# Optimization experiments

Hardware: AMD Instinct MI355X
Metric: run time of the kernel (lower is better)

The kernel has to match this reference:

```python
import jax, jax.numpy as jnp
import numpy as np

EMBED_DIM = 256
NUM_WEIGHTS = 8
NUM_RELATIONS = 5
BATCH = 131072


def setup_inputs() -> dict:
    key = jax.random.key(0)
    k1, k2, k3, k4 = jax.random.split(key, 4)
    embeds1 = jax.random.normal(k1, (BATCH, EMBED_DIM), dtype=jnp.float32)
    embeds2 = jax.random.normal(k2, (BATCH, EMBED_DIM), dtype=jnp.float32)
    # Embedding(num_weights, D*D): torch default init is N(0,1)
    rel_embeds = jax.random.normal(k3, (NUM_WEIGHTS, EMBED_DIM * EMBED_DIM), dtype=jnp.float32)
    # weight_scalars ~ U(-stdv, stdv), stdv = 1/sqrt(num_relations)
    stdv = 1.0 / np.sqrt(NUM_RELATIONS)
    weight_scalars = jax.random.uniform(
        k4, (NUM_WEIGHTS, NUM_RELATIONS), dtype=jnp.float32, minval=-stdv, maxval=stdv
    )
    return {
        "embeds1": embeds1,
        "embeds2": embeds2,
        "rel_embeds": rel_embeds,
        "weight_scalars": weight_scalars,
    }


def reference(embeds1, embeds2, rel_embeds, weight_scalars):
    D = embeds1.shape[1]
    W = rel_embeds.shape[0]
    rel_mats = rel_embeds.reshape(W, D, D)  # [W, D, D]
    # Fused bilinear form u . R_w . v for every w: [B, W]
    basis_outputs = jnp.einsum("bi,wij,bj->bw", embeds1, rel_mats, embeds2)
    logit = basis_outputs @ weight_scalars  # [B, R]
    return logit
```

## Files before the change

### kernel.cpp

```cpp
#include <hip/hip_runtime.h>
#include <hip/hip_bf16.h>

#define ED   256
#define NW   8
#define NR   5
#define BM   128
#define BCOL 128
#define BK   32
#define NSTEP (NR * 8)

typedef float  f32x4  __attribute__((ext_vector_type(4)));
typedef __bf16 bf16x8 __attribute__((ext_vector_type(8)));
typedef unsigned short u16;

__device__ __forceinline__ u16 f2bf(float f) {
    return __builtin_bit_cast(u16, __float2bfloat16(f));
}

__device__ __forceinline__ bf16x8 pack8(f32x4 a, f32x4 b) {
    union { u16 u[8]; bf16x8 v; } r;
    r.u[0] = f2bf(a[0]); r.u[1] = f2bf(a[1]); r.u[2] = f2bf(a[2]); r.u[3] = f2bf(a[3]);
    r.u[4] = f2bf(b[0]); r.u[5] = f2bf(b[1]); r.u[6] = f2bf(b[2]); r.u[7] = f2bf(b[3]);
    return r.v;
}

__global__ void prep_S(const float* __restrict__ rel,
                       const float* __restrict__ ws,
                       u16* __restrict__ S_T) {
    int idx = blockIdx.x * blockDim.x + threadIdx.x;
    if (idx >= ED * ED) return;
    int i = idx & (ED - 1);
    int j = idx >> 8;
    float acc[NR];
#pragma unroll
    for (int r = 0; r < NR; ++r) acc[r] = 0.f;
#pragma unroll
    for (int w = 0; w < NW; ++w) {
        float rv = rel[(size_t)w * ED * ED + (size_t)i * ED + j];
#pragma unroll
        for (int r = 0; r < NR; ++r) acc[r] += rv * ws[w * NR + r];
    }
#pragma unroll
    for (int r = 0; r < NR; ++r)
        S_T[((size_t)r * ED + j) * ED + i] = f2bf(acc[r]);
}

__global__ __launch_bounds__(256, 2) void bilinear_kernel(
    const float* __restrict__ e1, const float* __restrict__ e2,
    const u16* __restrict__ S_T, float* __restrict__ out) {

    __shared__ __align__(16) u16 Bbuf[4][BCOL * BK];
    __shared__ __align__(16) u16 E2l[BM * BCOL];
    __shared__ float Red[NR][BM][2];

    const int t    = threadIdx.x;
    const int wave = t >> 6;
    const int lane = t & 63;
    const int l15  = lane & 15;
    const int l4   = lane >> 4;
    const int wr   = wave >> 1;
    const int wc   = wave & 1;

    const int g       = blockIdx.x;
    const int per_xcd = gridDim.x >> 3;
    const int wgid    = (g & 7) * per_xcd + (g >> 3);
    const int ch      = wgid & 1;
    const long b0     = (long)(wgid >> 1) * BM;

    auto STAGE = [&](int rr, int kb, int b) {
        const u16* gb = S_T + ((size_t)rr * ED + ch * BCOL) * ED + kb * BK;
#pragma unroll
        for (int q = 0; q < 2; ++q) {
            int s2 = q * 256 + t;
            int j  = s2 >> 2;
            int c  = s2 & 3;
            int cl = c ^ ((j >> 1) & 3);
            const u16* gp = gb + (size_t)j * ED + cl * 8;
            u16* lp = &Bbuf[b][(size_t)(q * 256 + wave * 64) * 8];
            __builtin_amdgcn_global_load_lds(
                (const __attribute__((address_space(1))) unsigned int*)gp,
                (__attribute__((address_space(3))) unsigned int*)lp, 16, 0, 0);
        }
    };

    STAGE(0, 0, 0);
    STAGE(0, 1, 1);

#pragma unroll
    for (int q = 0; q < 16; ++q) {
        int idx = q * 256 + t;
        int row = idx >> 5;
        int c4  = idx & 31;
        f32x4 v = *(const f32x4*)(e2 + (b0 + row) * ED + ch * BCOL + c4 * 4);
        ushort4 p = make_ushort4(f2bf(v[0]), f2bf(v[1]), f2bf(v[2]), f2bf(v[3]));
        *(ushort4*)&E2l[row * BCOL + c4 * 4] = p;
    }

    bf16x8 av[4][8];
#pragma unroll
    for (int m = 0; m < 4; ++m) {
        const float* rowp = e1 + (b0 + wr * 64 + m * 16 + l15) * ED + l4 * 8;
#pragma unroll
        for (int kb = 0; kb < 8; ++kb) {
            f32x4 a = *(const f32x4*)(rowp + kb * 32);
            f32x4 b = *(const f32x4*)(rowp + kb * 32 + 4);
            av[m][kb] = pack8(a, b);
        }
    }

    asm volatile("s_waitcnt vmcnt(0) lgkmcnt(0)" ::: "memory");
    __builtin_amdgcn_s_barrier();

#pragma unroll
    for (int r = 0; r < NR; ++r) {
        f32x4 acc[4][4];
#pragma unroll
        for (int m = 0; m < 4; ++m)
#pragma unroll
            for (int n = 0; n < 4; ++n)
                acc[m][n] = f32x4{0.f, 0.f, 0.f, 0.f};

#pragma unroll
        for (int kb = 0; kb < 8; ++kb) {
            const int s = r * 8 + kb;

            if (s + 2 < NSTEP) {
                const int sn = s + 2;
                STAGE(sn >> 3, sn & 7, sn & 3);
            }

            if (s < NSTEP - 2)
                asm volatile("s_waitcnt vmcnt(4)" ::: "memory");
            else if (s == NSTEP - 2)
                asm volatile("s_waitcnt vmcnt(2)" ::: "memory");
            else
                asm volatile("s_waitcnt vmcnt(0)" ::: "memory");
            __builtin_amdgcn_s_barrier();
            __builtin_amdgcn_sched_barrier(0);

            bf16x8 bv[4];
#pragma unroll
            for (int n = 0; n < 4; ++n) {
                int j  = wc * 64 + n * 16 + l15;
                int lb = j * (BK * 2) + l4 * 16;
                int pb = lb ^ (((j >> 1) & 3) << 4);
                bv[n] = *(const bf16x8*)((const char*)Bbuf[s & 3] + pb);
            }
#pragma unroll
            for (int m = 0; m < 4; ++m)
#pragma unroll
                for (int n = 0; n < 4; ++n)
                    acc[m][n] = __builtin_amdgcn_mfma_f32_16x16x32_bf16(
                        av[m][kb], bv[n], acc[m][n], 0, 0, 0);
        }

#pragma unroll
        for (int m = 0; m < 4; ++m)
#pragma unroll
            for (int reg = 0; reg < 4; ++reg) {
                const int row = wr * 64 + m * 16 + l4 * 4 + reg;
                float p = 0.f;
#pragma unroll
                for (int n = 0; n < 4; ++n) {
                    unsigned bits =
                        (unsigned)E2l[row * BCOL + wc * 64 + n * 16 + l15] << 16;
                    p += acc[m][n][reg] * __builtin_bit_cast(float, bits);
                }
#pragma unroll
                for (int off = 1; off < 16; off <<= 1)
                    p += __shfl_xor(p, off);
                if (l15 == 0) Red[r][row][wc] = p;
            }
    }

    __syncthreads();
    for (int idx = t; idx < BM * NR; idx += 256) {
        int row = idx / NR;
        int r   = idx - row * NR;
        atomicAdd(&out[(b0 + row) * NR + r], Red[r][row][0] + Red[r][row][1]);
    }
}

extern "C" void kernel_launch(void* const* d_in, const int* in_sizes, int n_in,
                              void* d_out, int out_size, void* d_ws, size_t ws_size,
                              hipStream_t stream) {
    const float* e1  = (const float*)d_in[0];
    const float* e2  = (const float*)d_in[1];
    const float* rel = (const float*)d_in[2];
    const float* ws  = (const float*)d_in[3];
    float* out = (float*)d_out;
    u16* S_T = (u16*)d_ws;

    prep_S<<<(ED * ED + 255) / 256, 256, 0, stream>>>(rel, ws, S_T);

    hipMemsetAsync(out, 0, (size_t)out_size * sizeof(float), stream);

    int B = in_sizes[0] / ED;
    int grid = (B / BM) * 2;
    bilinear_kernel<<<grid, 256, 0, stream>>>(e1, e2, S_T, out);
}
```

Before: 217.6 us.

## Stage full-K relation tiles with 8-wave blocks and register-held e2

Doubles the workgroup to 512 threads (4x2 wave grid, each wave a 64x32 output slice). The S tile for a whole relation (all of K) is staged into a double-buffered LDS area, prefetching the next relation while computing the current one. This cuts the barriers from one per K-step to one per relation. The e2 values needed for the epilogue are loaded directly into packed registers instead of an LDS tile. The cost is a larger LDS footprint (128KB), which likely allows only one block per CU, plus more redundant e1 loading per wave.

```diff
diff --git a/kernel.cpp b/kernel.cpp
--- a/kernel.cpp
+++ b/kernel.cpp
@@ -6,8 +6,6 @@
 #define NR   5
 #define BM   128
 #define BCOL 128
-#define BK   32
-#define NSTEP (NR * 8)
 
 typedef float  f32x4  __attribute__((ext_vector_type(4)));
 typedef __bf16 bf16x8 __attribute__((ext_vector_type(8)));
@@ -45,21 +43,20 @@
         S_T[((size_t)r * ED + j) * ED + i] = f2bf(acc[r]);
 }
 
-__global__ __launch_bounds__(256, 2) void bilinear_kernel(
+__global__ __launch_bounds__(512, 2) void bilinear_kernel(
     const float* __restrict__ e1, const float* __restrict__ e2,
     const u16* __restrict__ S_T, float* __restrict__ out) {
 
-    __shared__ __align__(16) u16 Bbuf[4][BCOL * BK];
-    __shared__ __align__(16) u16 E2l[BM * BCOL];
-    __shared__ float Red[NR][BM][2];
+    __shared__ __align__(16) u16 Bbuf[2][BCOL * ED];
+    __shared__ float Red[NR][BM][4];
 
     const int t    = threadIdx.x;
     const int wave = t >> 6;
     const int lane = t & 63;
     const int l15  = lane & 15;
     const int l4   = lane >> 4;
-    const int wr   = wave >> 1;
-    const int wc   = wave & 1;
+    const int wr   = wave >> 2;
+    const int wc   = wave & 3;
 
     const int g       = blockIdx.x;
     const int per_xcd = gridDim.x >> 3;
@@ -67,34 +64,23 @@
     const int ch      = wgid & 1;
     const long b0     = (long)(wgid >> 1) * BM;
 
-    auto STAGE = [&](int rr, int kb, int b) {
-        const u16* gb = S_T + ((size_t)rr * ED + ch * BCOL) * ED + kb * BK;
+    auto STAGE = [&](int rr, int buf) {
+        const u16* gb = S_T + ((size_t)rr * ED + ch * BCOL) * ED;
 #pragma unroll
-        for (int q = 0; q < 2; ++q) {
-            int s2 = q * 256 + t;
-            int j  = s2 >> 2;
-            int c  = s2 & 3;
-            int cl = c ^ ((j >> 1) & 3);
+        for (int q = 0; q < 8; ++q) {
+            int idx = q * 512 + t;
+            int j   = idx >> 5;
+            int c   = idx & 31;
+            int cl  = c ^ (j & 7);
             const u16* gp = gb + (size_t)j * ED + cl * 8;
-            u16* lp = &Bbuf[b][(size_t)(q * 256 + wave * 64) * 8];
+            u16* lp = &Bbuf[buf][(size_t)(q * 512 + wave * 64) * 8];
             __builtin_amdgcn_global_load_lds(
                 (const __attribute__((address_space(1))) unsigned int*)gp,
                 (__attribute__((address_space(3))) unsigned int*)lp, 16, 0, 0);
         }
     };
 
-    STAGE(0, 0, 0);
-    STAGE(0, 1, 1);
-
-#pragma unroll
-    for (int q = 0; q < 16; ++q) {
-        int idx = q * 256 + t;
-        int row = idx >> 5;
-        int c4  = idx & 31;
-        f32x4 v = *(const f32x4*)(e2 + (b0 + row) * ED + ch * BCOL + c4 * 4);
-        ushort4 p = make_ushort4(f2bf(v[0]), f2bf(v[1]), f2bf(v[2]), f2bf(v[3]));
-        *(ushort4*)&E2l[row * BCOL + c4 * 4] = p;
-    }
+    STAGE(0, 0);
 
     bf16x8 av[4][8];
 #pragma unroll
@@ -108,48 +94,48 @@
         }
     }
 
-    asm volatile("s_waitcnt vmcnt(0) lgkmcnt(0)" ::: "memory");
+    unsigned e2p[4][4];
+#pragma unroll
+    for (int m = 0; m < 4; ++m)
+#pragma unroll
+        for (int reg = 0; reg < 4; ++reg) {
+            const float* erow =
+                e2 + (b0 + wr * 64 + m * 16 + l4 * 4 + reg) * ED
+                   + ch * BCOL + wc * 32 + l15;
+            float a = __builtin_nontemporal_load(erow);
+            float b = __builtin_nontemporal_load(erow + 16);
+            e2p[m][reg] = (unsigned)f2bf(a) | ((unsigned)f2bf(b) << 16);
+        }
+
+    asm volatile("s_waitcnt vmcnt(0)" ::: "memory");
     __builtin_amdgcn_s_barrier();
+    __builtin_amdgcn_sched_barrier(0);
 
 #pragma unroll
     for (int r = 0; r < NR; ++r) {
-        f32x4 acc[4][4];
+        if (r + 1 < NR) STAGE(r + 1, (r + 1) & 1);
+
+        f32x4 acc[4][2];
 #pragma unroll
         for (int m = 0; m < 4; ++m)
 #pragma unroll
-            for (int n = 0; n < 4; ++n)
+            for (int n = 0; n < 2; ++n)
                 acc[m][n] = f32x4{0.f, 0.f, 0.f, 0.f};
 
 #pragma unroll
         for (int kb = 0; kb < 8; ++kb) {
-            const int s = r * 8 + kb;
-
-            if (s + 2 < NSTEP) {
-                const int sn = s + 2;
-                STAGE(sn >> 3, sn & 7, sn & 3);
-            }
-
-            if (s < NSTEP - 2)
-                asm volatile("s_waitcnt vmcnt(4)" ::: "memory");
-            else if (s == NSTEP - 2)
-                asm volatile("s_waitcnt vmcnt(2)" ::: "memory");
-            else
-                asm volatile("s_waitcnt vmcnt(0)" ::: "memory");
-            __builtin_amdgcn_s_barrier();
-            __builtin_amdgcn_sched_barrier(0);
-
-            bf16x8 bv[4];
+            bf16x8 bv[2];
 #pragma unroll
-            for (int n = 0; n < 4; ++n) {
-                int j  = wc * 64 + n * 16 + l15;
-                int lb = j * (BK * 2) + l4 * 16;
-                int pb = lb ^ (((j >> 1) & 3) << 4);
-                bv[n] = *(const bf16x8*)((const char*)Bbuf[s & 3] + pb);
+            for (int n = 0; n < 2; ++n) {
+                int j  = wc * 32 + n * 16 + l15;
+                int c  = (kb * 4 + l4) ^ (j & 7);
+                bv[n] = *(const bf16x8*)
+                    ((const char*)Bbuf[r & 1] + ((size_t)j * 32 + c) * 16);
             }
 #pragma unroll
             for (int m = 0; m < 4; ++m)
 #pragma unroll
-                for (int n = 0; n < 4; ++n)
+                for (int n = 0; n < 2; ++n)
                     acc[m][n] = __builtin_amdgcn_mfma_f32_16x16x32_bf16(
                         av[m][kb], bv[n], acc[m][n], 0, 0, 0);
         }
@@ -159,25 +145,29 @@
 #pragma unroll
             for (int reg = 0; reg < 4; ++reg) {
                 const int row = wr * 64 + m * 16 + l4 * 4 + reg;
-                float p = 0.f;
-#pragma unroll
-                for (int n = 0; n < 4; ++n) {
-                    unsigned bits =
-                        (unsigned)E2l[row * BCOL + wc * 64 + n * 16 + l15] << 16;
-                    p += acc[m][n][reg] * __builtin_bit_cast(float, bits);
-                }
+                unsigned u = e2p[m][reg];
+                float p = acc[m][0][reg] *
+                              __builtin_bit_cast(float, u << 16) +
+                          acc[m][1][reg] *
+                              __builtin_bit_cast(float, u & 0xffff0000u);
 #pragma unroll
                 for (int off = 1; off < 16; off <<= 1)
                     p += __shfl_xor(p, off);
                 if (l15 == 0) Red[r][row][wc] = p;
             }
+
+        asm volatile("s_waitcnt vmcnt(0)" ::: "memory");
+        __builtin_amdgcn_s_barrier();
+        __builtin_amdgcn_sched_barrier(0);
     }
 
     __syncthreads();
-    for (int idx = t; idx < BM * NR; idx += 256) {
+    for (int idx = t; idx < BM * NR; idx += 512) {
         int row = idx / NR;
         int r   = idx - row * NR;
-        atomicAdd(&out[(b0 + row) * NR + r], Red[r][row][0] + Red[r][row][1]);
+        atomicAdd(&out[(b0 + row) * NR + r],
+                  Red[r][row][0] + Red[r][row][1] +
+                  Red[r][row][2] + Red[r][row][3]);
     }
 }
 
@@ -197,5 +187,5 @@
 
     int B = in_sizes[0] / ED;
     int grid = (B / BM) * 2;
-    bilinear_kernel<<<grid, 256, 0, stream>>>(e1, e2, S_T, out);
+    bilinear_kernel<<<grid, 512, 0, stream>>>(e1, e2, S_T, out);
 }
```

Result: slower. 340.4 us (+56.4%).

## Double K tile size, drop e2 LDS staging, and raise MFMA priority

Applied to the files above, without the earlier changes.

Raises the B-tile K depth from 32 to 64, halving the number of pipeline steps and barriers, and switches to an 8-way XOR swizzle suited to the wider rows. The bf16 copy of e2 in LDS is removed, and the epilogue reads e2 straight from global memory in fp32. This frees LDS that may allow more occupancy, and s_setprio is raised around the MFMA block. In exchange, the epilogue now makes scattered global loads of e2 for every reduction step, and the larger stages double LDS use per buffer.

```diff
diff --git a/kernel.cpp b/kernel.cpp
--- a/kernel.cpp
+++ b/kernel.cpp
@@ -6,8 +6,8 @@
 #define NR   5
 #define BM   128
 #define BCOL 128
-#define BK   32
-#define NSTEP (NR * 8)
+#define BK   64
+#define NSTEP (NR * 4)
 
 typedef float  f32x4  __attribute__((ext_vector_type(4)));
 typedef __bf16 bf16x8 __attribute__((ext_vector_type(8)));
@@ -50,7 +50,6 @@
     const u16* __restrict__ S_T, float* __restrict__ out) {
 
     __shared__ __align__(16) u16 Bbuf[4][BCOL * BK];
-    __shared__ __align__(16) u16 E2l[BM * BCOL];
     __shared__ float Red[NR][BM][2];
 
     const int t    = threadIdx.x;
@@ -70,11 +69,11 @@
     auto STAGE = [&](int rr, int kb, int b) {
         const u16* gb = S_T + ((size_t)rr * ED + ch * BCOL) * ED + kb * BK;
 #pragma unroll
-        for (int q = 0; q < 2; ++q) {
+        for (int q = 0; q < 4; ++q) {
             int s2 = q * 256 + t;
-            int j  = s2 >> 2;
-            int c  = s2 & 3;
-            int cl = c ^ ((j >> 1) & 3);
+            int j  = s2 >> 3;
+            int c  = s2 & 7;
+            int cl = c ^ (j & 7);
             const u16* gp = gb + (size_t)j * ED + cl * 8;
             u16* lp = &Bbuf[b][(size_t)(q * 256 + wave * 64) * 8];
             __builtin_amdgcn_global_load_lds(
@@ -85,16 +84,6 @@
 
     STAGE(0, 0, 0);
     STAGE(0, 1, 1);
-
-#pragma unroll
-    for (int q = 0; q < 16; ++q) {
-        int idx = q * 256 + t;
-        int row = idx >> 5;
-        int c4  = idx & 31;
-        f32x4 v = *(const f32x4*)(e2 + (b0 + row) * ED + ch * BCOL + c4 * 4);
-        ushort4 p = make_ushort4(f2bf(v[0]), f2bf(v[1]), f2bf(v[2]), f2bf(v[3]));
-        *(ushort4*)&E2l[row * BCOL + c4 * 4] = p;
-    }
 
     bf16x8 av[4][8];
 #pragma unroll
@@ -108,7 +97,7 @@
         }
     }
 
-    asm volatile("s_waitcnt vmcnt(0) lgkmcnt(0)" ::: "memory");
+    asm volatile("s_waitcnt vmcnt(0)" ::: "memory");
     __builtin_amdgcn_s_barrier();
 
 #pragma unroll
@@ -121,37 +110,42 @@
                 acc[m][n] = f32x4{0.f, 0.f, 0.f, 0.f};
 
 #pragma unroll
-        for (int kb = 0; kb < 8; ++kb) {
-            const int s = r * 8 + kb;
+        for (int kb = 0; kb < 4; ++kb) {
+            const int s = r * 4 + kb;
 
             if (s + 2 < NSTEP) {
                 const int sn = s + 2;
-                STAGE(sn >> 3, sn & 7, sn & 3);
+                STAGE(sn >> 2, sn & 3, sn & 3);
             }
 
             if (s < NSTEP - 2)
+                asm volatile("s_waitcnt vmcnt(8)" ::: "memory");
+            else if (s == NSTEP - 2)
                 asm volatile("s_waitcnt vmcnt(4)" ::: "memory");
-            else if (s == NSTEP - 2)
-                asm volatile("s_waitcnt vmcnt(2)" ::: "memory");
             else
                 asm volatile("s_waitcnt vmcnt(0)" ::: "memory");
             __builtin_amdgcn_s_barrier();
             __builtin_amdgcn_sched_barrier(0);
 
-            bf16x8 bv[4];
+            __builtin_amdgcn_s_setprio(1);
 #pragma unroll
-            for (int n = 0; n < 4; ++n) {
-                int j  = wc * 64 + n * 16 + l15;
-                int lb = j * (BK * 2) + l4 * 16;
-                int pb = lb ^ (((j >> 1) & 3) << 4);
-                bv[n] = *(const bf16x8*)((const char*)Bbuf[s & 3] + pb);
+            for (int h = 0; h < 2; ++h) {
+                bf16x8 bv[4];
+#pragma unroll
+                for (int n = 0; n < 4; ++n) {
+                    int j  = wc * 64 + n * 16 + l15;
+                    int lb = j * (BK * 2) + h * 64 + l4 * 16;
+                    int pb = lb ^ ((j & 7) << 4);
+                    bv[n] = *(const bf16x8*)((const char*)Bbuf[s & 3] + pb);
+                }
+#pragma unroll
+                for (int m = 0; m < 4; ++m)
+#pragma unroll
+                    for (int n = 0; n < 4; ++n)
+                        acc[m][n] = __builtin_amdgcn_mfma_f32_16x16x32_bf16(
+                            av[m][kb * 2 + h], bv[n], acc[m][n], 0, 0, 0);
             }
-#pragma unroll
-            for (int m = 0; m < 4; ++m)
-#pragma unroll
-                for (int n = 0; n < 4; ++n)
-                    acc[m][n] = __builtin_amdgcn_mfma_f32_16x16x32_bf16(
-                        av[m][kb], bv[n], acc[m][n], 0, 0, 0);
+            __builtin_amdgcn_s_setprio(0);
         }
 
 #pragma unroll
@@ -159,13 +153,12 @@
 #pragma unroll
             for (int reg = 0; reg < 4; ++reg) {
                 const int row = wr * 64 + m * 16 + l4 * 4 + reg;
+                const float* er =
+                    e2 + (b0 + row) * ED + ch * BCOL + wc * 64 + l15;
                 float p = 0.f;
 #pragma unroll
-                for (int n = 0; n < 4; ++n) {
-                    unsigned bits =
-                        (unsigned)E2l[row * BCOL + wc * 64 + n * 16 + l15] << 16;
-                    p += acc[m][n][reg] * __builtin_bit_cast(float, bits);
-                }
+                for (int n = 0; n < 4; ++n)
+                    p += acc[m][n][reg] * er[n * 16];
 #pragma unroll
                 for (int off = 1; off < 16; off <<= 1)
                     p += __shfl_xor(p, off);
```

After: 366.1 us. 68.2% more time.
